# Kernel optimization log

Hardware: AMD Instinct MI355X
Metric: run time of the kernel (lower is better)

Reference implementation:

```python
import jax, jax.numpy as jnp
import numpy as np

B, T, C = 4, 2048, 1024
H = 16
D = C // H  # head_size = 64


def setup_inputs() -> dict:
    key = jax.random.key(0)
    ks = jax.random.split(key, 9)
    s = 1.0 / np.sqrt(C).astype(np.float32)
    return {
        "x": jax.random.normal(ks[0], (B, T, C), dtype=jnp.float32),
        "Wq": jax.random.normal(ks[1], (C, C), dtype=jnp.float32) * s,
        "bq": jnp.zeros((C,), dtype=jnp.float32),
        "Wk": jax.random.normal(ks[2], (C, C), dtype=jnp.float32) * s,
        "bk": jnp.zeros((C,), dtype=jnp.float32),
        "Wv": jax.random.normal(ks[3], (C, C), dtype=jnp.float32) * s,
        "bv": jnp.zeros((C,), dtype=jnp.float32),
        "Wp": jax.random.normal(ks[4], (C, C), dtype=jnp.float32) * s,
        "bp": jnp.zeros((C,), dtype=jnp.float32),
    }


def reference(x, Wq, bq, Wk, bk, Wv, bv, Wp, bp):
    # Linear projections, then split heads: (B, T, C) -> (B, H, T, D)
    def heads(t):
        return t.reshape(B, T, H, D).transpose(0, 2, 1, 3)

    q = heads(x @ Wq + bq)
    k = heads(x @ Wk + bk)
    v = heads(x @ Wv + bv)

    scale = 1.0 / np.sqrt(D).astype(np.float32)
    att = jnp.einsum("bhqd,bhkd->bhqk", q, k) * scale  # (B, H, T, T)
    att = jax.nn.softmax(att, axis=-1)
    y = jnp.einsum("bhqk,bhkd->bhqd", att, v)  # (B, H, T, D)
    y = y.transpose(0, 2, 1, 3).reshape(B, T, C)
    return y @ Wp + bp
```

## Files before the change

kernel.cpp:

```cpp
#include <hip/hip_runtime.h>

typedef unsigned int uint;
typedef unsigned short ushort;

typedef __bf16 bf16x8 __attribute__((ext_vector_type(8)));
typedef __bf16 bf16x2 __attribute__((ext_vector_type(2)));
typedef float f32x4 __attribute__((ext_vector_type(4)));
typedef float f32x16 __attribute__((ext_vector_type(16)));
typedef uint uint2v __attribute__((ext_vector_type(2)));

union U4 { uint4 u; bf16x8 v; };
union UB2 { bf16x2 v; uint u; };

__device__ __forceinline__ ushort f2bf(float f){
  uint u = __float_as_uint(f);
  u += 0x7fffu + ((u >> 16) & 1u);
  return (ushort)(u >> 16);
}

__device__ __forceinline__ uint packbf(float lo, float hi){
  UB2 t; t.v[0] = (__bf16)lo; t.v[1] = (__bf16)hi;
  return t.u;
}

__device__ __forceinline__ float exp2a(float x){
  float r; asm("v_exp_f32 %0, %1" : "=v"(r) : "v"(x)); return r;
}

__device__ __forceinline__ void gload16(const void* g, void* l){
  __builtin_amdgcn_global_load_lds((const __attribute__((address_space(1))) uint*)g,
                                   (__attribute__((address_space(3))) uint*)l, 16, 0, 0);
}

__device__ __forceinline__ f32x16 mfma32(U4 a, U4 b, f32x16 c){
  return __builtin_amdgcn_mfma_f32_32x32x16_bf16(a.v, b.v, c, 0, 0, 0);
}

__global__ __launch_bounds__(256, 2) void gemm_bt(
    const ushort* __restrict__ Ahp, const ushort* __restrict__ Bhp,
    const float* __restrict__ bias, void* __restrict__ outp,
    int mode, float oscale)
{
  __shared__ uint4 smem4[2048];
  char* sAh = (char*)smem4;
  char* sBh = (char*)smem4 + 16384;

  const int tid  = threadIdx.x;
  const int lane = tid & 63;
  const int wid  = tid >> 6;
  const int wm = (wid >> 1) * 64;
  const int wn = (wid & 1) * 64;

  int lin = blockIdx.y * 64 + blockIdx.x;
  int xcd = lin & 7, j = lin >> 3;
  const long tm = (long)(xcd * 8 + (j & 7)) * 128;
  const long tn = (long)(j >> 3) * 128;

  const char* gA = (const char*)Ahp;
  const char* gB = (const char*)Bhp;

  f32x4 acc[4][4] = {};

  for (int ks = 0; ks < 16; ks++){
    const int koff = ks * 128;
    #pragma unroll
    for (int c = 0; c < 4; c++){
      int o   = (tid + 256*c) * 16;
      int row = o >> 7;
      int src = (o & 127) ^ ((row & 7) << 4);
      gload16(gA + (tm + row)*2048 + koff + src, sAh + o);
      gload16(gB + (tn + row)*2048 + koff + src, sBh + o);
    }
    __syncthreads();
    #pragma unroll
    for (int k = 0; k < 2; k++){
      const int kb = k*64 + (lane >> 4)*16;
      U4 ah[4], bh[4];
      #pragma unroll
      for (int m = 0; m < 4; m++){
        int row = wm + m*16 + (lane & 15);
        ah[m].u = *(const uint4*)(sAh + row*128 + (kb ^ ((row & 7) << 4)));
      }
      #pragma unroll
      for (int n = 0; n < 4; n++){
        int row = wn + n*16 + (lane & 15);
        bh[n].u = *(const uint4*)(sBh + row*128 + (kb ^ ((row & 7) << 4)));
      }
      __builtin_amdgcn_s_setprio(1);
      #pragma unroll
      for (int m = 0; m < 4; m++)
      #pragma unroll
      for (int n = 0; n < 4; n++)
        acc[m][n] = __builtin_amdgcn_mfma_f32_16x16x32_bf16(ah[m].v, bh[n].v, acc[m][n], 0,0,0);
      __builtin_amdgcn_s_setprio(0);
    }
    __syncthreads();
  }

  #pragma unroll
  for (int n = 0; n < 4; n++){
    int colg = (int)tn + wn + n*16 + (lane & 15);
    float bv = bias[colg];
    #pragma unroll
    for (int m = 0; m < 4; m++){
      int rowg0 = (int)tm + wm + m*16 + ((lane >> 4) * 4);
      float v0 = (acc[m][n][0] + bv) * oscale;
      float v1 = (acc[m][n][1] + bv) * oscale;
      float v2 = (acc[m][n][2] + bv) * oscale;
      float v3 = (acc[m][n][3] + bv) * oscale;
      if (mode == 0){
        ushort* o = (ushort*)outp;
        o[(long)(rowg0+0)*1024 + colg] = f2bf(v0);
        o[(long)(rowg0+1)*1024 + colg] = f2bf(v1);
        o[(long)(rowg0+2)*1024 + colg] = f2bf(v2);
        o[(long)(rowg0+3)*1024 + colg] = f2bf(v3);
      } else if (mode == 1){
        int b = rowg0 >> 11, t0 = rowg0 & 2047;
        int h = colg >> 6, d = colg & 63;
        ushort4 o4;
        o4.x = f2bf(v0); o4.y = f2bf(v1); o4.z = f2bf(v2); o4.w = f2bf(v3);
        *(ushort4*)&((ushort*)outp)[(((long)(b*16 + h))*64 + d)*2048 + t0] = o4;
      } else {
        float* o = (float*)outp;
        o[(long)(rowg0+0)*1024 + colg] = v0;
        o[(long)(rowg0+1)*1024 + colg] = v1;
        o[(long)(rowg0+2)*1024 + colg] = v2;
        o[(long)(rowg0+3)*1024 + colg] = v3;
      }
    }
  }
}

__device__ __forceinline__ void mkfrag(const uint (&pk)[8], U4 (&out)[2])
{
  #pragma unroll
  for (int kl = 0; kl < 2; kl++){
    int bb = kl*4;
    uint2v r02 = __builtin_amdgcn_permlane32_swap(pk[bb+0], pk[bb+2], false, false);
    uint2v r13 = __builtin_amdgcn_permlane32_swap(pk[bb+1], pk[bb+3], false, false);
    out[kl].u = make_uint4(r02[0], r13[0], r02[1], r13[1]);
  }
}

__global__ __launch_bounds__(256, 2) void attn_kernel(
    const ushort* __restrict__ Qg, const ushort* __restrict__ Kg,
    const ushort* __restrict__ Vtg, ushort* __restrict__ Yg)
{
  __shared__ uint4 smem[2048];
  char* sK0 = (char*)smem;
  char* sV0 = (char*)smem + 8192;
  char* sK1 = (char*)smem + 16384;
  char* sV1 = (char*)smem + 24576;

  const int tid  = threadIdx.x;
  const int lane = tid & 63;
  const int w    = tid >> 6;
  const int ql   = lane & 31;
  const int hh   = lane >> 5;

  int lin = blockIdx.y * 8 + blockIdx.x;
  int xcd = lin & 7, jj = lin >> 3;
  const int bh  = (jj >> 3) * 8 + xcd;
  const int qb  = jj & 7;
  const int tq0 = qb * 256 + w * 64;
  const int b = bh >> 4, h = bh & 15;

  U4 qf[2][4];
  #pragma unroll
  for (int g = 0; g < 2; g++){
    const char* qrow = (const char*)Qg + (long)(b*2048 + tq0 + g*32 + ql)*2048 + h*128 + hh*16;
    #pragma unroll
    for (int c = 0; c < 4; c++) qf[g][c].u = *(const uint4*)(qrow + c*32);
  }

  f32x16 y00 = {}, y01 = {}, y10 = {}, y11 = {};
  float ls0 = 0.f, ls1 = 0.f;

  const char* kbase = (const char*)Kg  + (long)b*2048*2048 + h*128;
  const char* vbase = (const char*)Vtg + (long)bh*64*4096;

  auto stage = [&](char* dK, char* dV, int kc){
    #pragma unroll
    for (int c2 = 0; c2 < 2; c2++){
      int o   = tid*16 + c2*4096;
      int row = o >> 7;
      int src = (o & 127) ^ ((row & 7) << 4);
      gload16(kbase + (long)(kc*64 + row)*2048 + src, dK + o);
      gload16(vbase + (long)row*4096 + (long)kc*128 + src, dV + o);
    }
  };

  auto sm = [&](f32x16& s, float& ls, uint (&pk)[8]){
    float ps = 0.f;
    #pragma unroll
    for (int r = 0; r < 16; r++){ s[r] = exp2a(s[r]); ps += s[r]; }
    ls += ps;
    #pragma unroll
    for (int i = 0; i < 8; i++) pk[i] = packbf(s[2*i], s[2*i+1]);
  };

  auto body = [&](int kc, char* cK, char* cV, char* nK, char* nV){
    if (kc < 31){
      stage(nK, nV, kc + 1);
      asm volatile("s_waitcnt vmcnt(4)" ::: "memory");
    } else {
      asm volatile("s_waitcnt vmcnt(0)" ::: "memory");
    }
    __builtin_amdgcn_s_barrier();

    f32x16 s00 = {}, s10 = {};
    __builtin_amdgcn_s_setprio(1);
    #pragma unroll
    for (int ksd = 0; ksd < 4; ksd++){
      int kb = ksd*32 + hh*16;
      int r = ql;
      U4 a; a.u = *(const uint4*)(cK + r*128 + (kb ^ ((r & 7) << 4)));
      s00 = mfma32(a, qf[0][ksd], s00);
      s10 = mfma32(a, qf[1][ksd], s10);
    }
    __builtin_amdgcn_s_setprio(0);

    uint pk00[8], pk10[8];
    sm(s00, ls0, pk00); sm(s10, ls1, pk10);
    U4 f0[2], f1[2];
    mkfrag(pk00, f0); mkfrag(pk10, f1);

    f32x16 s01 = {}, s11 = {};
    __builtin_amdgcn_s_setprio(1);
    #pragma unroll
    for (int ksd = 0; ksd < 4; ksd++){
      int kb = ksd*32 + hh*16;
      int r = 32 + ql;
      U4 a; a.u = *(const uint4*)(cK + r*128 + (kb ^ ((r & 7) << 4)));
      s01 = mfma32(a, qf[0][ksd], s01);
      s11 = mfma32(a, qf[1][ksd], s11);
    }

    #pragma unroll
    for (int kl = 0; kl < 2; kl++){
      int kvo = kl*32 + hh*16;
      U4 a0, a1;
      { int r = ql;      a0.u = *(const uint4*)(cV + r*128 + (kvo ^ ((r & 7) << 4))); }
      { int r = 32 + ql; a1.u = *(const uint4*)(cV + r*128 + (kvo ^ ((r & 7) << 4))); }
      y00 = mfma32(a0, f0[kl], y00);
      y01 = mfma32(a1, f0[kl], y01);
      y10 = mfma32(a0, f1[kl], y10);
      y11 = mfma32(a1, f1[kl], y11);
    }
    __builtin_amdgcn_s_setprio(0);

    uint pk01[8], pk11[8];
    sm(s01, ls0, pk01); sm(s11, ls1, pk11);
    mkfrag(pk01, f0); mkfrag(pk11, f1);

    __builtin_amdgcn_s_setprio(1);
    #pragma unroll
    for (int kl = 0; kl < 2; kl++){
      int kvo = 64 + kl*32 + hh*16;
      U4 a0, a1;
      { int r = ql;      a0.u = *(const uint4*)(cV + r*128 + (kvo ^ ((r & 7) << 4))); }
      { int r = 32 + ql; a1.u = *(const uint4*)(cV + r*128 + (kvo ^ ((r & 7) << 4))); }
      y00 = mfma32(a0, f0[kl], y00);
      y01 = mfma32(a1, f0[kl], y01);
      y10 = mfma32(a0, f1[kl], y10);
      y11 = mfma32(a1, f1[kl], y11);
    }
    __builtin_amdgcn_s_setprio(0);

    if (kc < 31){
      asm volatile("" ::: "memory");
      __builtin_amdgcn_s_barrier();
    }
  };

  stage(sK0, sV0, 0);
  for (int kc2 = 0; kc2 < 16; kc2++){
    body(2*kc2 + 0, sK0, sV0, sK1, sV1);
    body(2*kc2 + 1, sK1, sV1, sK0, sV0);
  }

  #pragma unroll
  for (int g = 0; g < 2; g++){
    f32x16& t0 = g ? y10 : y00;
    f32x16& t1 = g ? y11 : y01;
    float ls   = g ? ls1 : ls0;
    float lt   = ls + __shfl_xor(ls, 32);
    float inv  = 1.0f / lt;
    int tq = tq0 + g*32 + ql;
    ushort* yrow = Yg + ((long)b*2048 + tq)*1024 + h*64;
    #pragma unroll
    for (int qi = 0; qi < 4; qi++){
      ushort4 o0, o1;
      o0.x = f2bf(t0[qi*4+0]*inv); o0.y = f2bf(t0[qi*4+1]*inv);
      o0.z = f2bf(t0[qi*4+2]*inv); o0.w = f2bf(t0[qi*4+3]*inv);
      o1.x = f2bf(t1[qi*4+0]*inv); o1.y = f2bf(t1[qi*4+1]*inv);
      o1.z = f2bf(t1[qi*4+2]*inv); o1.w = f2bf(t1[qi*4+3]*inv);
      *(ushort4*)(yrow + qi*8 + hh*4)      = o0;
      *(ushort4*)(yrow + 32 + qi*8 + hh*4) = o1;
    }
  }
}

__global__ void cast_x_kernel(const float* __restrict__ x, ushort* __restrict__ xh)
{
  int i = blockIdx.x*256 + threadIdx.x;
  float4 v = ((const float4*)x)[i];
  ushort4 h;
  h.x = f2bf(v.x); h.y = f2bf(v.y); h.z = f2bf(v.z); h.w = f2bf(v.w);
  ((ushort4*)xh)[i] = h;
}

__global__ void wsplit_kernel(const float* __restrict__ W, ushort* __restrict__ Th)
{
  __shared__ float tile[64][65];
  const int tid = threadIdx.x;
  const int k0 = blockIdx.x * 64;
  const int n0 = blockIdx.y * 64;
  #pragma unroll
  for (int c = 0; c < 4; c++){
    int idx = tid + 256*c;
    int r = idx >> 4, c4 = idx & 15;
    float4 v = *(const float4*)&W[(long)(k0 + r)*1024 + n0 + c4*4];
    tile[r][c4*4+0] = v.x; tile[r][c4*4+1] = v.y;
    tile[r][c4*4+2] = v.z; tile[r][c4*4+3] = v.w;
  }
  __syncthreads();
  #pragma unroll
  for (int c = 0; c < 4; c++){
    int idx = tid + 256*c;
    int nr = idx >> 4, k4 = idx & 15;
    ushort4 hh;
    hh.x = f2bf(tile[k4*4+0][nr]); hh.y = f2bf(tile[k4*4+1][nr]);
    hh.z = f2bf(tile[k4*4+2][nr]); hh.w = f2bf(tile[k4*4+3][nr]);
    *(ushort4*)&Th[(long)(n0 + nr)*1024 + k0 + k4*4] = hh;
  }
}

extern "C" void kernel_launch(void* const* d_in, const int* in_sizes, int n_in,
                              void* d_out, int out_size, void* d_ws, size_t ws_size,
                              hipStream_t stream)
{
  const float* x  = (const float*)d_in[0];
  const float* Wq = (const float*)d_in[1];
  const float* bq = (const float*)d_in[2];
  const float* Wk = (const float*)d_in[3];
  const float* bk = (const float*)d_in[4];
  const float* Wv = (const float*)d_in[5];
  const float* bv = (const float*)d_in[6];
  const float* Wp = (const float*)d_in[7];
  const float* bp = (const float*)d_in[8];

  char* ws = (char*)d_ws;
  const size_t SZ_X = 16777216;
  const size_t SZ_W = 2097152;
  ushort* xh  = (ushort*)(ws);
  ushort* wqh = (ushort*)(ws + SZ_X);
  ushort* wkh = (ushort*)(ws + SZ_X + 1*SZ_W);
  ushort* wvh = (ushort*)(ws + SZ_X + 2*SZ_W);
  ushort* wph = (ushort*)(ws + SZ_X + 3*SZ_W);
  ushort* Qb  = (ushort*)(ws + SZ_X + 4*SZ_W);
  ushort* Kb  = (ushort*)(ws + 2*SZ_X + 4*SZ_W);
  ushort* Vtb = (ushort*)(ws + 3*SZ_X + 4*SZ_W);
  ushort* Yb  = (ushort*)(ws + 4*SZ_X + 4*SZ_W);

  cast_x_kernel<<<8192, 256, 0, stream>>>(x, xh);
  dim3 wg(16, 16);
  wsplit_kernel<<<wg, 256, 0, stream>>>(Wq, wqh);
  wsplit_kernel<<<wg, 256, 0, stream>>>(Wk, wkh);
  wsplit_kernel<<<wg, 256, 0, stream>>>(Wv, wvh);
  wsplit_kernel<<<wg, 256, 0, stream>>>(Wp, wph);

  dim3 gg(64, 8);
  gemm_bt<<<gg, 256, 0, stream>>>(xh, wqh, bq, Qb, 0, 0.18033688f);
  gemm_bt<<<gg, 256, 0, stream>>>(xh, wkh, bk, Kb, 0, 1.0f);
  gemm_bt<<<gg, 256, 0, stream>>>(xh, wvh, bv, Vtb, 1, 1.0f);

  dim3 ag(8, 64);
  attn_kernel<<<ag, 256, 0, stream>>>(Qb, Kb, Vtb, Yb);

  gemm_bt<<<gg, 256, 0, stream>>>(Yb, wph, bp, d_out, 2, 1.0f);
}
```

Baseline: 288.8 us.

## Double-buffer GEMM loads and halve attention rows per wave for occupancy

The projection GEMM now stages the next K-slice into a second 32 KB LDS buffer while computing the current one, with partial vmcnt waits instead of full syncthreads, so global loads overlap MFMA work. Separately, the attention kernel now gives each wave 32 query rows instead of 64, doubles the grid and raises launch bounds to 4 blocks per CU. This cuts register pressure to raise occupancy, but each K/V tile loaded into LDS is reused by fewer queries. The doubled GEMM LDS footprint (64 KB) may limit its occupancy.

Result: slower. 304.2 us (+5.3%).

```diff
diff --git a/kernel.cpp b/kernel.cpp
--- a/kernel.cpp
+++ b/kernel.cpp
@@ -41,9 +41,8 @@
     const float* __restrict__ bias, void* __restrict__ outp,
     int mode, float oscale)
 {
-  __shared__ uint4 smem4[2048];
-  char* sAh = (char*)smem4;
-  char* sBh = (char*)smem4 + 16384;
+  __shared__ uint4 smem4[4096];
+  char* sm = (char*)smem4;
 
   const int tid  = threadIdx.x;
   const int lane = tid & 63;
@@ -61,17 +60,32 @@
 
   f32x4 acc[4][4] = {};
 
-  for (int ks = 0; ks < 16; ks++){
+  auto stage = [&](char* buf, int ks){
     const int koff = ks * 128;
     #pragma unroll
     for (int c = 0; c < 4; c++){
       int o   = (tid + 256*c) * 16;
       int row = o >> 7;
       int src = (o & 127) ^ ((row & 7) << 4);
-      gload16(gA + (tm + row)*2048 + koff + src, sAh + o);
-      gload16(gB + (tn + row)*2048 + koff + src, sBh + o);
-    }
-    __syncthreads();
+      gload16(gA + (tm + row)*2048 + koff + src, buf + o);
+      gload16(gB + (tn + row)*2048 + koff + src, buf + 16384 + o);
+    }
+  };
+
+  stage(sm, 0);
+  for (int ks = 0; ks < 16; ks++){
+    char* cur = sm + (ks & 1) * 32768;
+    char* nxt = sm + ((ks + 1) & 1) * 32768;
+    if (ks < 15){
+      stage(nxt, ks + 1);
+      asm volatile("s_waitcnt vmcnt(8)" ::: "memory");
+    } else {
+      asm volatile("s_waitcnt vmcnt(0)" ::: "memory");
+    }
+    __builtin_amdgcn_s_barrier();
+
+    char* sAh = cur;
+    char* sBh = cur + 16384;
     #pragma unroll
     for (int k = 0; k < 2; k++){
       const int kb = k*64 + (lane >> 4)*16;
@@ -94,7 +108,8 @@
         acc[m][n] = __builtin_amdgcn_mfma_f32_16x16x32_bf16(ah[m].v, bh[n].v, acc[m][n], 0,0,0);
       __builtin_amdgcn_s_setprio(0);
     }
-    __syncthreads();
+    asm volatile("" ::: "memory");
+    __builtin_amdgcn_s_barrier();
   }
 
   #pragma unroll
@@ -142,7 +157,7 @@
   }
 }
 
-__global__ __launch_bounds__(256, 2) void attn_kernel(
+__global__ __launch_bounds__(256, 4) void attn_kernel(
     const ushort* __restrict__ Qg, const ushort* __restrict__ Kg,
     const ushort* __restrict__ Vtg, ushort* __restrict__ Yg)
 {
@@ -158,23 +173,20 @@
   const int ql   = lane & 31;
   const int hh   = lane >> 5;
 
-  int lin = blockIdx.y * 8 + blockIdx.x;
-  int xcd = lin & 7, jj = lin >> 3;
-  const int bh  = (jj >> 3) * 8 + xcd;
-  const int qb  = jj & 7;
-  const int tq0 = qb * 256 + w * 64;
+  int lin = blockIdx.y * 16 + blockIdx.x;
+  int xcd = lin & 7, j = lin >> 3;
+  const int bh  = (j >> 4) * 8 + xcd;
+  const int qb  = j & 15;
+  const int tq0 = qb * 128 + w * 32;
   const int b = bh >> 4, h = bh & 15;
 
-  U4 qf[2][4];
-  #pragma unroll
-  for (int g = 0; g < 2; g++){
-    const char* qrow = (const char*)Qg + (long)(b*2048 + tq0 + g*32 + ql)*2048 + h*128 + hh*16;
-    #pragma unroll
-    for (int c = 0; c < 4; c++) qf[g][c].u = *(const uint4*)(qrow + c*32);
-  }
-
-  f32x16 y00 = {}, y01 = {}, y10 = {}, y11 = {};
-  float ls0 = 0.f, ls1 = 0.f;
+  U4 qf[4];
+  const char* qrow = (const char*)Qg + (long)(b*2048 + tq0 + ql)*2048 + h*128 + hh*16;
+  #pragma unroll
+  for (int c = 0; c < 4; c++) qf[c].u = *(const uint4*)(qrow + c*32);
+
+  f32x16 y0 = {}, y1 = {};
+  float ls = 0.f;
 
   const char* kbase = (const char*)Kg  + (long)b*2048*2048 + h*128;
   const char* vbase = (const char*)Vtg + (long)bh*64*4096;
@@ -190,7 +202,7 @@
     }
   };
 
-  auto sm = [&](f32x16& s, float& ls, uint (&pk)[8]){
+  auto sm = [&](f32x16& s, uint (&pk)[8]){
     float ps = 0.f;
     #pragma unroll
     for (int r = 0; r < 16; r++){ s[r] = exp2a(s[r]); ps += s[r]; }
@@ -208,62 +220,37 @@
     }
     __builtin_amdgcn_s_barrier();
 
-    f32x16 s00 = {}, s10 = {};
+    f32x16 s0 = {}, s1 = {};
     __builtin_amdgcn_s_setprio(1);
     #pragma unroll
     for (int ksd = 0; ksd < 4; ksd++){
       int kb = ksd*32 + hh*16;
-      int r = ql;
-      U4 a; a.u = *(const uint4*)(cK + r*128 + (kb ^ ((r & 7) << 4)));
-      s00 = mfma32(a, qf[0][ksd], s00);
-      s10 = mfma32(a, qf[1][ksd], s10);
+      U4 a0, a1;
+      { int r = ql;      a0.u = *(const uint4*)(cK + r*128 + (kb ^ ((r & 7) << 4))); }
+      { int r = 32 + ql; a1.u = *(const uint4*)(cK + r*128 + (kb ^ ((r & 7) << 4))); }
+      s0 = mfma32(a0, qf[ksd], s0);
+      s1 = mfma32(a1, qf[ksd], s1);
     }
     __builtin_amdgcn_s_setprio(0);
 
-    uint pk00[8], pk10[8];
-    sm(s00, ls0, pk00); sm(s10, ls1, pk10);
+    uint pk0[8], pk1[8];
+    sm(s0, pk0); sm(s1, pk1);
     U4 f0[2], f1[2];
-    mkfrag(pk00, f0); mkfrag(pk10, f1);
-
-    f32x16 s01 = {}, s11 = {};
+    mkfrag(pk0, f0); mkfrag(pk1, f1);
+
     __builtin_amdgcn_s_setprio(1);
     #pragma unroll
-    for (int ksd = 0; ksd < 4; ksd++){
-      int kb = ksd*32 + hh*16;
-      int r = 32 + ql;
-      U4 a; a.u = *(const uint4*)(cK + r*128 + (kb ^ ((r & 7) << 4)));
-      s01 = mfma32(a, qf[0][ksd], s01);
-      s11 = mfma32(a, qf[1][ksd], s11);
-    }
-
-    #pragma unroll
-    for (int kl = 0; kl < 2; kl++){
-      int kvo = kl*32 + hh*16;
-      U4 a0, a1;
-      { int r = ql;      a0.u = *(const uint4*)(cV + r*128 + (kvo ^ ((r & 7) << 4))); }
-      { int r = 32 + ql; a1.u = *(const uint4*)(cV + r*128 + (kvo ^ ((r & 7) << 4))); }
-      y00 = mfma32(a0, f0[kl], y00);
-      y01 = mfma32(a1, f0[kl], y01);
-      y10 = mfma32(a0, f1[kl], y10);
-      y11 = mfma32(a1, f1[kl], y11);
-    }
-    __builtin_amdgcn_s_setprio(0);
-
-    uint pk01[8], pk11[8];
-    sm(s01, ls0, pk01); sm(s11, ls1, pk11);
-    mkfrag(pk01, f0); mkfrag(pk11, f1);
-
-    __builtin_amdgcn_s_setprio(1);
-    #pragma unroll
-    for (int kl = 0; kl < 2; kl++){
-      int kvo = 64 + kl*32 + hh*16;
-      U4 a0, a1;
-      { int r = ql;      a0.u = *(const uint4*)(cV + r*128 + (kvo ^ ((r & 7) << 4))); }
-      { int r = 32 + ql; a1.u = *(const uint4*)(cV + r*128 + (kvo ^ ((r & 7) << 4))); }
-      y00 = mfma32(a0, f0[kl], y00);
-      y01 = mfma32(a1, f0[kl], y01);
-      y10 = mfma32(a0, f1[kl], y10);
-      y11 = mfma32(a1, f1[kl], y11);
+    for (int n = 0; n < 2; n++){
+      #pragma unroll
+      for (int kl = 0; kl < 2; kl++){
+        int kvo = n*64 + kl*32 + hh*16;
+        U4 a0, a1;
+        { int r = ql;      a0.u = *(const uint4*)(cV + r*128 + (kvo ^ ((r & 7) << 4))); }
+        { int r = 32 + ql; a1.u = *(const uint4*)(cV + r*128 + (kvo ^ ((r & 7) << 4))); }
+        U4 bb = n ? f1[kl] : f0[kl];
+        y0 = mfma32(a0, bb, y0);
+        y1 = mfma32(a1, bb, y1);
+      }
     }
     __builtin_amdgcn_s_setprio(0);
 
@@ -279,25 +266,19 @@
     body(2*kc2 + 1, sK1, sV1, sK0, sV0);
   }
 
-  #pragma unroll
-  for (int g = 0; g < 2; g++){
-    f32x16& t0 = g ? y10 : y00;
-    f32x16& t1 = g ? y11 : y01;
-    float ls   = g ? ls1 : ls0;
-    float lt   = ls + __shfl_xor(ls, 32);
-    float inv  = 1.0f / lt;
-    int tq = tq0 + g*32 + ql;
-    ushort* yrow = Yg + ((long)b*2048 + tq)*1024 + h*64;
-    #pragma unroll
-    for (int qi = 0; qi < 4; qi++){
-      ushort4 o0, o1;
-      o0.x = f2bf(t0[qi*4+0]*inv); o0.y = f2bf(t0[qi*4+1]*inv);
-      o0.z = f2bf(t0[qi*4+2]*inv); o0.w = f2bf(t0[qi*4+3]*inv);
-      o1.x = f2bf(t1[qi*4+0]*inv); o1.y = f2bf(t1[qi*4+1]*inv);
-      o1.z = f2bf(t1[qi*4+2]*inv); o1.w = f2bf(t1[qi*4+3]*inv);
-      *(ushort4*)(yrow + qi*8 + hh*4)      = o0;
-      *(ushort4*)(yrow + 32 + qi*8 + hh*4) = o1;
-    }
+  float lt  = ls + __shfl_xor(ls, 32);
+  float inv = 1.0f / lt;
+  int tq = tq0 + ql;
+  ushort* yrow = Yg + ((long)b*2048 + tq)*1024 + h*64;
+  #pragma unroll
+  for (int qi = 0; qi < 4; qi++){
+    ushort4 o0, o1;
+    o0.x = f2bf(y0[qi*4+0]*inv); o0.y = f2bf(y0[qi*4+1]*inv);
+    o0.z = f2bf(y0[qi*4+2]*inv); o0.w = f2bf(y0[qi*4+3]*inv);
+    o1.x = f2bf(y1[qi*4+0]*inv); o1.y = f2bf(y1[qi*4+1]*inv);
+    o1.z = f2bf(y1[qi*4+2]*inv); o1.w = f2bf(y1[qi*4+3]*inv);
+    *(ushort4*)(yrow + qi*8 + hh*4)      = o0;
+    *(ushort4*)(yrow + 32 + qi*8 + hh*4) = o1;
   }
 }
 
@@ -375,7 +356,7 @@
   gemm_bt<<<gg, 256, 0, stream>>>(xh, wkh, bk, Kb, 0, 1.0f);
   gemm_bt<<<gg, 256, 0, stream>>>(xh, wvh, bv, Vtb, 1, 1.0f);
 
-  dim3 ag(8, 64);
+  dim3 ag(16, 64);
   attn_kernel<<<ag, 256, 0, stream>>>(Qb, Kb, Vtb, Yb);
 
   gemm_bt<<<gg, 256, 0, stream>>>(Yb, wph, bp, d_out, 2, 1.0f);
```
